# Optimization experiments

Measured on AMD Instinct MI355X. Metric: run time of the kernel, lower is better.

The kernel has to match this reference:

```python
import jax, jax.numpy as jnp
import numpy as np
import jax.ops

N_NODES = 50000
N_EDGES = 800000
N_GRAPHS = 512
F_IN = 128
HID = 256
N_CLASSES = 1

def _xavier(key, shape):
    fan_in, fan_out = shape[0], shape[1]
    std = (2.0 / (fan_in + fan_out)) ** 0.5
    return jax.random.normal(key, shape, dtype=jnp.float32) * std

def setup_inputs() -> dict:
    key = jax.random.key(0)
    ks = jax.random.split(key, 12)
    x = jax.random.normal(ks[0], (N_NODES, F_IN), dtype=jnp.float32)
    edge_index = jax.random.randint(ks[1], (2, N_EDGES), 0, N_NODES, dtype=jnp.int64)
    batch = jnp.sort(jax.random.randint(ks[2], (N_NODES,), 0, N_GRAPHS, dtype=jnp.int64))
    return {
        'x': x, 'edge_index': edge_index, 'batch': batch,
        'W0': _xavier(ks[3], (F_IN, HID)), 'b0': jnp.zeros((HID,), jnp.float32),
        'W1': _xavier(ks[4], (HID, HID)), 'b1': jnp.zeros((HID,), jnp.float32),
        'W2': _xavier(ks[5], (HID, HID)), 'b2': jnp.zeros((HID,), jnp.float32),
        'Wm1': _xavier(ks[6], (HID, HID)), 'bm1': jnp.zeros((HID,), jnp.float32),
        'Wm2': _xavier(ks[7], (HID, N_CLASSES)), 'bm2': jnp.zeros((N_CLASSES,), jnp.float32),
    }

def _gcn_layer(h, W, b, src, dst, deg_inv_sqrt):
    # PyG GCNConv: linear -> symmetric-normalized aggregation (with self loops) -> bias
    hw = h @ W                                        # [N, out]
    norm = deg_inv_sqrt[src] * deg_inv_sqrt[dst]      # [E]
    msg = hw[src] * norm[:, None]                     # [E, out]
    agg = jax.ops.segment_sum(msg, dst, num_segments=N_NODES)
    agg = agg + hw * (deg_inv_sqrt ** 2)[:, None]     # self-loop term
    return agg + b

def reference(x, edge_index, batch, W0, b0, W1, b1, W2, b2, Wm1, bm1, Wm2, bm2):
    src, dst = edge_index[0], edge_index[1]
    # degree with added self loops (in-degree at dst)
    deg = jax.ops.segment_sum(jnp.ones((N_EDGES,), jnp.float32), dst, num_segments=N_NODES) + 1.0
    deg_inv_sqrt = jax.lax.rsqrt(deg)
    h = jax.nn.relu(_gcn_layer(x, W0, b0, src, dst, deg_inv_sqrt))
    h = jax.nn.relu(_gcn_layer(h, W1, b1, src, dst, deg_inv_sqrt))
    h = jax.nn.relu(_gcn_layer(h, W2, b2, src, dst, deg_inv_sqrt))
    # global mean pool over graphs
    sums = jax.ops.segment_sum(h, batch, num_segments=N_GRAPHS)
    cnts = jax.ops.segment_sum(jnp.ones((N_NODES,), jnp.float32), batch, num_segments=N_GRAPHS)
    pooled = sums / jnp.maximum(cnts, 1.0)[:, None]   # [G, HID]
    out = jax.nn.relu(pooled @ Wm1 + bm1) @ Wm2 + bm2 # [G, num_classes]
    return out
```

## Files before the change

### kernel.cpp

```cpp
#include <hip/hip_runtime.h>

constexpr int N_NODES  = 50000;
constexpr int N_EDGES  = 800000;
constexpr int N_GRAPHS = 512;
constexpr int F_IN     = 128;
constexpr int HID      = 256;
constexpr int NPAD     = 50048;

typedef short short8 __attribute__((ext_vector_type(8)));
typedef float f32x4  __attribute__((ext_vector_type(4)));

__device__ __forceinline__ unsigned short f2b(float f) {
    unsigned u = __float_as_uint(f);
    u += 0x7fffu + ((u >> 16) & 1u);
    return (unsigned short)(u >> 16);
}
__device__ __forceinline__ float b2f_lo(unsigned u) { return __uint_as_float(u << 16); }
__device__ __forceinline__ float b2f_hi(unsigned u) { return __uint_as_float(u & 0xffff0000u); }

__global__ __launch_bounds__(256) void prep_kernel(
    const int* __restrict__ dst, int* __restrict__ deg,
    const float* __restrict__ x, unsigned short* __restrict__ x_bf,
    const float* __restrict__ W0, const float* __restrict__ W1, const float* __restrict__ W2,
    unsigned short* __restrict__ Wt0, unsigned short* __restrict__ Wt1, unsigned short* __restrict__ Wt2)
{
    const int b = blockIdx.x, t = threadIdx.x;
    if (b < 3125) {
        int e = b * 256 + t;
        atomicAdd(&deg[dst[e]], 1);
    } else if (b < 9375) {
        int i = (b - 3125) * 256 + t;
        float4 v = *reinterpret_cast<const float4*>(x + (size_t)i * 4);
        unsigned r0 = (unsigned)f2b(v.x) | ((unsigned)f2b(v.y) << 16);
        unsigned r1 = (unsigned)f2b(v.z) | ((unsigned)f2b(v.w) << 16);
        *reinterpret_cast<uint2*>(x_bf + (size_t)i * 4) = make_uint2(r0, r1);
    } else {
        int i = (b - 9375) * 256 + t;
        const float* W; unsigned short* Wt; int K; int j;
        if (i < 32768)      { W = W0; Wt = Wt0; K = 128; j = i; }
        else if (i < 98304) { W = W1; Wt = Wt1; K = 256; j = i - 32768; }
        else                { W = W2; Wt = Wt2; K = 256; j = i - 98304; }
        int k = j >> 8, n = j & 255;
        int idx = (n >> 7) * (K * 128) + (((k >> 3) * 128 + (n & 127)) << 3) + (k & 7);
        Wt[idx] = f2b(W[j]);
    }
}

__global__ void block_sum_dis_kernel(const int* __restrict__ deg, int* __restrict__ bsum,
                                     float* __restrict__ dis, int n) {
    __shared__ int sm[256];
    int t = threadIdx.x, base = blockIdx.x * 1024;
    int s = 0;
    #pragma unroll
    for (int i = 0; i < 4; ++i) {
        int idx = base + t + i * 256;
        if (idx < n) { int d = deg[idx]; s += d; dis[idx] = rsqrtf((float)d + 1.0f); }
    }
    sm[t] = s; __syncthreads();
    for (int o = 128; o > 0; o >>= 1) { if (t < o) sm[t] += sm[t + o]; __syncthreads(); }
    if (t == 0) bsum[blockIdx.x] = sm[0];
}

__global__ void scan_bsum_kernel(int* __restrict__ bsum, int nb) {
    __shared__ int sm[64];
    int t = threadIdx.x;
    int v = (t < nb) ? bsum[t] : 0;
    sm[t] = v; __syncthreads();
    for (int o = 1; o < 64; o <<= 1) {
        int a = (t >= o) ? sm[t - o] : 0; __syncthreads();
        sm[t] += a; __syncthreads();
    }
    if (t < nb) bsum[t] = sm[t] - v;
}

__global__ void scan_local_kernel(const int* __restrict__ deg, const int* __restrict__ bsum,
                                  int* __restrict__ row_start, int* __restrict__ cursor, int n) {
    __shared__ int sm[256];
    int t = threadIdx.x, base = blockIdx.x * 1024;
    int idx0 = base + t * 4;
    int v[4], s = 0;
    #pragma unroll
    for (int i = 0; i < 4; ++i) { int id = idx0 + i; v[i] = (id < n) ? deg[id] : 0; s += v[i]; }
    sm[t] = s; __syncthreads();
    for (int o = 1; o < 256; o <<= 1) {
        int a = (t >= o) ? sm[t - o] : 0; __syncthreads();
        sm[t] += a; __syncthreads();
    }
    int excl = bsum[blockIdx.x] + sm[t] - s;
    #pragma unroll
    for (int i = 0; i < 4; ++i) {
        int id = idx0 + i;
        if (id < n) { row_start[id] = excl; cursor[id] = excl; }
        excl += v[i];
    }
    if (blockIdx.x == gridDim.x - 1 && t == 255) row_start[n] = excl;
}

__global__ void fill_csr(const int* __restrict__ src, const int* __restrict__ dst,
                         const float* __restrict__ dis, int* __restrict__ cursor,
                         int2* __restrict__ csr) {
    int e = blockIdx.x * blockDim.x + threadIdx.x;
    if (e >= N_EDGES) return;
    int s = src[e], d = dst[e];
    int pos = atomicAdd(&cursor[d], 1);
    float w = dis[s] * dis[d];
    csr[pos] = make_int2(s, __float_as_int(w));
}

template<int F>
__global__ __launch_bounds__(256) void agg_bf16(
    const unsigned short* __restrict__ hin, const int* __restrict__ row_start,
    const int2* __restrict__ csr, const float* __restrict__ dis,
    uint4* __restrict__ out4)
{
    constexpr int LPR  = F / 8;
    constexpr int NSUB = 64 / LPR;
    const int lane = threadIdx.x & 63;
    const int sub  = lane / LPR;
    const int fc   = lane % LPR;
    const int node = blockIdx.x * 4 + (threadIdx.x >> 6);
    if (node >= N_NODES) return;

    float acc[8];
    {
        float dn = dis[node];
        float sw = (sub == 0) ? dn * dn : 0.0f;
        uint2 u2[2];
        *reinterpret_cast<uint4*>(u2) =
            *reinterpret_cast<const uint4*>(hin + (size_t)node * F + fc * 8);
        #pragma unroll
        for (int h = 0; h < 2; ++h) {
            acc[h * 4 + 0] = b2f_lo(u2[h].x) * sw;
            acc[h * 4 + 1] = b2f_hi(u2[h].x) * sw;
            acc[h * 4 + 2] = b2f_lo(u2[h].y) * sw;
            acc[h * 4 + 3] = b2f_hi(u2[h].y) * sw;
        }
    }

    int j = row_start[node] + sub;
    const int end = row_start[node + 1];
    for (; j + 3 * NSUB < end; j += 4 * NSUB) {
        int2 c[4];
        #pragma unroll
        for (int u = 0; u < 4; ++u) c[u] = csr[j + u * NSUB];
        #pragma unroll
        for (int u = 0; u < 4; ++u) {
            float w = __int_as_float(c[u].y);
            uint2 g[2];
            *reinterpret_cast<uint4*>(g) =
                *reinterpret_cast<const uint4*>(hin + (size_t)c[u].x * F + fc * 8);
            #pragma unroll
            for (int h = 0; h < 2; ++h) {
                acc[h * 4 + 0] = fmaf(b2f_lo(g[h].x), w, acc[h * 4 + 0]);
                acc[h * 4 + 1] = fmaf(b2f_hi(g[h].x), w, acc[h * 4 + 1]);
                acc[h * 4 + 2] = fmaf(b2f_lo(g[h].y), w, acc[h * 4 + 2]);
                acc[h * 4 + 3] = fmaf(b2f_hi(g[h].y), w, acc[h * 4 + 3]);
            }
        }
    }
    for (; j < end; j += NSUB) {
        int2 c0 = csr[j];
        float w = __int_as_float(c0.y);
        uint2 g[2];
        *reinterpret_cast<uint4*>(g) =
            *reinterpret_cast<const uint4*>(hin + (size_t)c0.x * F + fc * 8);
        #pragma unroll
        for (int h = 0; h < 2; ++h) {
            acc[h * 4 + 0] = fmaf(b2f_lo(g[h].x), w, acc[h * 4 + 0]);
            acc[h * 4 + 1] = fmaf(b2f_hi(g[h].x), w, acc[h * 4 + 1]);
            acc[h * 4 + 2] = fmaf(b2f_lo(g[h].y), w, acc[h * 4 + 2]);
            acc[h * 4 + 3] = fmaf(b2f_hi(g[h].y), w, acc[h * 4 + 3]);
        }
    }

    #pragma unroll
    for (int k = 0; k < 8; ++k) {
        #pragma unroll
        for (int off = LPR; off < 64; off <<= 1)
            acc[k] += __shfl_xor(acc[k], off, 64);
    }

    if (sub == 0) {
        uint2 r[2];
        #pragma unroll
        for (int h = 0; h < 2; ++h) {
            r[h].x = (unsigned)f2b(acc[h * 4 + 0]) | ((unsigned)f2b(acc[h * 4 + 1]) << 16);
            r[h].y = (unsigned)f2b(acc[h * 4 + 2]) | ((unsigned)f2b(acc[h * 4 + 3]) << 16);
        }
        int chunk = (node >> 7) * (128 * (F / 8)) + fc * 128 + (node & 127);
        out4[chunk] = *reinterpret_cast<uint4*>(r);
    }
}

template<int K>
__global__ __launch_bounds__(256) void gemm_frag(
    const uint4* __restrict__ A4,
    const unsigned short* __restrict__ Wt_frag,
    const float* __restrict__ bias,
    unsigned short* __restrict__ C,
    int relu)
{
    __shared__ __align__(16) unsigned short Bs[K * 128];
    const int t    = threadIdx.x;
    const int lane = t & 63;
    const int w    = t >> 6;
    const int wm   = w & 1, wn = w >> 1;
    const int q    = lane >> 4, m = lane & 15;
    const int panel = blockIdx.x;
    const int col0  = blockIdx.y * 128;

    {
        const uint4* src4 = reinterpret_cast<const uint4*>(Wt_frag + blockIdx.y * (K * 128));
        uint4* dst4 = reinterpret_cast<uint4*>(Bs);
        #pragma unroll
        for (int it = 0; it < K / 16; ++it)
            dst4[it * 256 + t] = src4[it * 256 + t];
    }
    __syncthreads();

    f32x4 acc[4][4] = {};
    const int abase = panel * (128 * (K / 8));

    #pragma unroll
    for (int kb = 0; kb < K / 32; ++kb) {
        short8 af[4], bf[4];
        #pragma unroll
        for (int i = 0; i < 4; ++i) {
            uint4 v = A4[abase + (kb * 4 + q) * 128 + wm * 64 + i * 16 + m];
            af[i] = *reinterpret_cast<short8*>(&v);
        }
        #pragma unroll
        for (int jn = 0; jn < 4; ++jn)
            bf[jn] = *reinterpret_cast<const short8*>(&Bs[((kb * 4 + q) * 128 + wn * 64 + jn * 16 + m) * 8]);
        #pragma unroll
        for (int i = 0; i < 4; ++i)
            #pragma unroll
            for (int jn = 0; jn < 4; ++jn)
                acc[i][jn] = __builtin_amdgcn_mfma_f32_16x16x32_bf16(af[i], bf[jn], acc[i][jn], 0, 0, 0);
    }

    #pragma unroll
    for (int jn = 0; jn < 4; ++jn) {
        int col = col0 + wn * 64 + jn * 16 + m;
        float bj = bias[col];
        #pragma unroll
        for (int i = 0; i < 4; ++i) {
            int rowb = panel * 128 + wm * 64 + i * 16 + q * 4;
            #pragma unroll
            for (int r = 0; r < 4; ++r) {
                float v = acc[i][jn][r] + bj;
                if (relu) v = fmaxf(v, 0.f);
                C[(size_t)(rowb + r) * 256 + col] = f2b(v);
            }
        }
    }
}

__global__ __launch_bounds__(256) void pool_mlp_kernel(
    const unsigned short* __restrict__ h, const int* __restrict__ batch,
    const float* __restrict__ Wm1, const float* __restrict__ bm1,
    const float* __restrict__ Wm2, const float* __restrict__ bm2,
    float* __restrict__ out)
{
    __shared__ float p[HID];
    __shared__ float red[HID];
    __shared__ int se[2];
    const int g = blockIdx.x, t = threadIdx.x;
    if (t < 2) {
        int target = g + t;
        int lo = 0, hi = N_NODES;
        while (lo < hi) { int mid = (lo + hi) >> 1; if (batch[mid] < target) lo = mid + 1; else hi = mid; }
        se[t] = lo;
    }
    __syncthreads();
    const int s = se[0], e = se[1];
    float acc = 0.f;
    for (int n = s; n < e; ++n) acc += b2f_lo((unsigned)h[(size_t)n * HID + t]);
    p[t] = acc / fmaxf((float)(e - s), 1.0f);
    __syncthreads();
    float a2 = bm1[t];
    for (int k = 0; k < HID; ++k) a2 = fmaf(p[k], Wm1[k * HID + t], a2);
    red[t] = fmaxf(a2, 0.f) * Wm2[t];
    __syncthreads();
    for (int o = 128; o > 0; o >>= 1) {
        if (t < o) red[t] += red[t + o];
        __syncthreads();
    }
    if (t == 0) out[g] = red[0] + bm2[0];
}

extern "C" void kernel_launch(void* const* d_in, const int* in_sizes, int n_in,
                              void* d_out, int out_size, void* d_ws, size_t ws_size,
                              hipStream_t stream) {
    const float* x    = (const float*)d_in[0];
    const int*   ei   = (const int*)d_in[1];
    const int*   batch= (const int*)d_in[2];
    const float* W0   = (const float*)d_in[3];
    const float* b0   = (const float*)d_in[4];
    const float* W1   = (const float*)d_in[5];
    const float* b1   = (const float*)d_in[6];
    const float* W2   = (const float*)d_in[7];
    const float* b2   = (const float*)d_in[8];
    const float* Wm1  = (const float*)d_in[9];
    const float* bm1  = (const float*)d_in[10];
    const float* Wm2  = (const float*)d_in[11];
    const float* bm2  = (const float*)d_in[12];
    float* out = (float*)d_out;

    char* ws = (char*)d_ws;
    size_t off = 0;
    auto alloc = [&](size_t bytes) -> void* {
        void* p = ws + off;
        off += (bytes + 255) & ~(size_t)255;
        return p;
    };
    int*   deg       = (int*)  alloc((size_t)N_NODES * 4);
    float* dis       = (float*)alloc((size_t)N_NODES * 4);
    int*   row_start = (int*)  alloc((size_t)(N_NODES + 1) * 4);
    int*   cursor    = (int*)  alloc((size_t)N_NODES * 4);
    int*   bsum      = (int*)  alloc((size_t)64 * 4);
    int2*  csr       = (int2*) alloc((size_t)N_EDGES * 8);
    unsigned short* x_bf = (unsigned short*)alloc((size_t)N_NODES * F_IN * 2);
    unsigned short* Wt0  = (unsigned short*)alloc((size_t)F_IN * HID * 2);
    unsigned short* Wt1  = (unsigned short*)alloc((size_t)HID * HID * 2);
    unsigned short* Wt2  = (unsigned short*)alloc((size_t)HID * HID * 2);
    unsigned short* bufA = (unsigned short*)alloc((size_t)NPAD * HID * 2);
    unsigned short* bufB = (unsigned short*)alloc((size_t)NPAD * HID * 2);

    const int* src = ei;
    const int* dst = ei + N_EDGES;
    const int NB = (N_NODES + 1023) / 1024;

    hipMemsetAsync(deg, 0, (size_t)N_NODES * 4, stream);
    prep_kernel         <<<10015, 256, 0, stream>>>(dst, deg, x, x_bf, W0, W1, W2, Wt0, Wt1, Wt2);
    block_sum_dis_kernel<<<NB, 256, 0, stream>>>(deg, bsum, dis, N_NODES);
    scan_bsum_kernel    <<<1, 64, 0, stream>>>(bsum, NB);
    scan_local_kernel   <<<NB, 256, 0, stream>>>(deg, bsum, row_start, cursor, N_NODES);
    fill_csr            <<<(N_EDGES + 255) / 256, 256, 0, stream>>>(src, dst, dis, cursor, csr);

    dim3 ggrid(NPAD / 128, 2);

    agg_bf16<F_IN><<<(N_NODES + 3) / 4, 256, 0, stream>>>(x_bf, row_start, csr, dis, (uint4*)bufA);
    gemm_frag<F_IN><<<ggrid, 256, 0, stream>>>((const uint4*)bufA, Wt0, b0, bufB, 1);

    agg_bf16<HID><<<(N_NODES + 3) / 4, 256, 0, stream>>>(bufB, row_start, csr, dis, (uint4*)bufA);
    gemm_frag<HID><<<ggrid, 256, 0, stream>>>((const uint4*)bufA, Wt1, b1, bufB, 1);

    agg_bf16<HID><<<(N_NODES + 3) / 4, 256, 0, stream>>>(bufB, row_start, csr, dis, (uint4*)bufA);
    gemm_frag<HID><<<ggrid, 256, 0, stream>>>((const uint4*)bufA, Wt2, b2, bufB, 1);

    pool_mlp_kernel<<<N_GRAPHS, HID, 0, stream>>>(bufB, batch, Wm1, bm1, Wm2, bm2, out);
}
```

Baseline: 430.9 us.

## Fuse neighbor aggregation and MFMA GEMM per layer via swizzled LDS tile

Merges the separate aggregation and GEMM kernels into one per-layer kernel. Each block aggregates 64 node rows into a bank-swizzled LDS tile, then multiplies that tile by the full weight matrix with MFMA, reading B fragments directly from global memory. This removes the intermediate global round-trip and three kernel launches. In exchange, each wave aggregates 16 nodes sequentially, so there is less parallelism during the gather, and weights are read from global/L2 per block instead of being staged in shared memory.

```diff
diff --git a/kernel.cpp b/kernel.cpp
--- a/kernel.cpp
+++ b/kernel.cpp
@@ -107,150 +107,140 @@
     csr[pos] = make_int2(s, __float_as_int(w));
 }
 
-template<int F>
-__global__ __launch_bounds__(256) void agg_bf16(
-    const unsigned short* __restrict__ hin, const int* __restrict__ row_start,
-    const int2* __restrict__ csr, const float* __restrict__ dis,
-    uint4* __restrict__ out4)
+template<int K>
+__global__ __launch_bounds__(256, 4) void layer_fused(
+    const unsigned short* __restrict__ hin,
+    const int* __restrict__ row_start, const int2* __restrict__ csr,
+    const float* __restrict__ dis,
+    const unsigned short* __restrict__ Wfrag,
+    const float* __restrict__ bias,
+    unsigned short* __restrict__ hout)
 {
-    constexpr int LPR  = F / 8;
+    constexpr int CPR  = K / 8;
+    constexpr int LPR  = K / 8;
     constexpr int NSUB = 64 / LPR;
-    const int lane = threadIdx.x & 63;
-    const int sub  = lane / LPR;
-    const int fc   = lane % LPR;
-    const int node = blockIdx.x * 4 + (threadIdx.x >> 6);
-    if (node >= N_NODES) return;
-
-    float acc[8];
-    {
-        float dn = dis[node];
-        float sw = (sub == 0) ? dn * dn : 0.0f;
-        uint2 u2[2];
-        *reinterpret_cast<uint4*>(u2) =
-            *reinterpret_cast<const uint4*>(hin + (size_t)node * F + fc * 8);
-        #pragma unroll
-        for (int h = 0; h < 2; ++h) {
-            acc[h * 4 + 0] = b2f_lo(u2[h].x) * sw;
-            acc[h * 4 + 1] = b2f_hi(u2[h].x) * sw;
-            acc[h * 4 + 2] = b2f_lo(u2[h].y) * sw;
-            acc[h * 4 + 3] = b2f_hi(u2[h].y) * sw;
-        }
-    }
-
-    int j = row_start[node] + sub;
-    const int end = row_start[node + 1];
-    for (; j + 3 * NSUB < end; j += 4 * NSUB) {
-        int2 c[4];
-        #pragma unroll
-        for (int u = 0; u < 4; ++u) c[u] = csr[j + u * NSUB];
-        #pragma unroll
-        for (int u = 0; u < 4; ++u) {
-            float w = __int_as_float(c[u].y);
-            uint2 g[2];
-            *reinterpret_cast<uint4*>(g) =
-                *reinterpret_cast<const uint4*>(hin + (size_t)c[u].x * F + fc * 8);
-            #pragma unroll
-            for (int h = 0; h < 2; ++h) {
-                acc[h * 4 + 0] = fmaf(b2f_lo(g[h].x), w, acc[h * 4 + 0]);
-                acc[h * 4 + 1] = fmaf(b2f_hi(g[h].x), w, acc[h * 4 + 1]);
-                acc[h * 4 + 2] = fmaf(b2f_lo(g[h].y), w, acc[h * 4 + 2]);
-                acc[h * 4 + 3] = fmaf(b2f_hi(g[h].y), w, acc[h * 4 + 3]);
-            }
-        }
-    }
-    for (; j < end; j += NSUB) {
-        int2 c0 = csr[j];
-        float w = __int_as_float(c0.y);
-        uint2 g[2];
-        *reinterpret_cast<uint4*>(g) =
-            *reinterpret_cast<const uint4*>(hin + (size_t)c0.x * F + fc * 8);
-        #pragma unroll
-        for (int h = 0; h < 2; ++h) {
-            acc[h * 4 + 0] = fmaf(b2f_lo(g[h].x), w, acc[h * 4 + 0]);
-            acc[h * 4 + 1] = fmaf(b2f_hi(g[h].x), w, acc[h * 4 + 1]);
-            acc[h * 4 + 2] = fmaf(b2f_lo(g[h].y), w, acc[h * 4 + 2]);
-            acc[h * 4 + 3] = fmaf(b2f_hi(g[h].y), w, acc[h * 4 + 3]);
-        }
-    }
-
-    #pragma unroll
-    for (int k = 0; k < 8; ++k) {
-        #pragma unroll
-        for (int off = LPR; off < 64; off <<= 1)
-            acc[k] += __shfl_xor(acc[k], off, 64);
-    }
-
-    if (sub == 0) {
-        uint2 r[2];
-        #pragma unroll
-        for (int h = 0; h < 2; ++h) {
-            r[h].x = (unsigned)f2b(acc[h * 4 + 0]) | ((unsigned)f2b(acc[h * 4 + 1]) << 16);
-            r[h].y = (unsigned)f2b(acc[h * 4 + 2]) | ((unsigned)f2b(acc[h * 4 + 3]) << 16);
-        }
-        int chunk = (node >> 7) * (128 * (F / 8)) + fc * 128 + (node & 127);
-        out4[chunk] = *reinterpret_cast<uint4*>(r);
-    }
-}
-
-template<int K>
-__global__ __launch_bounds__(256) void gemm_frag(
-    const uint4* __restrict__ A4,
-    const unsigned short* __restrict__ Wt_frag,
-    const float* __restrict__ bias,
-    unsigned short* __restrict__ C,
-    int relu)
-{
-    __shared__ __align__(16) unsigned short Bs[K * 128];
+    __shared__ __align__(16) uint4 Alds[64 * CPR];
+
     const int t    = threadIdx.x;
     const int lane = t & 63;
     const int w    = t >> 6;
-    const int wm   = w & 1, wn = w >> 1;
-    const int q    = lane >> 4, m = lane & 15;
     const int panel = blockIdx.x;
-    const int col0  = blockIdx.y * 128;
-
-    {
-        const uint4* src4 = reinterpret_cast<const uint4*>(Wt_frag + blockIdx.y * (K * 128));
-        uint4* dst4 = reinterpret_cast<uint4*>(Bs);
-        #pragma unroll
-        for (int it = 0; it < K / 16; ++it)
-            dst4[it * 256 + t] = src4[it * 256 + t];
+    const int sub  = lane / LPR;
+    const int fc   = lane % LPR;
+
+    for (int nn = 0; nn < 16; ++nn) {
+        const int r    = w * 16 + nn;
+        const int node = panel * 64 + r;
+        float acc[8];
+        if (node < N_NODES) {
+            {
+                float dn = dis[node];
+                float sw = (sub == 0) ? dn * dn : 0.0f;
+                uint2 u2[2];
+                *reinterpret_cast<uint4*>(u2) =
+                    *reinterpret_cast<const uint4*>(hin + (size_t)node * K + fc * 8);
+                #pragma unroll
+                for (int h = 0; h < 2; ++h) {
+                    acc[h * 4 + 0] = b2f_lo(u2[h].x) * sw;
+                    acc[h * 4 + 1] = b2f_hi(u2[h].x) * sw;
+                    acc[h * 4 + 2] = b2f_lo(u2[h].y) * sw;
+                    acc[h * 4 + 3] = b2f_hi(u2[h].y) * sw;
+                }
+            }
+            int j = row_start[node] + sub;
+            const int end = row_start[node + 1];
+            for (; j + 3 * NSUB < end; j += 4 * NSUB) {
+                int2 c[4];
+                #pragma unroll
+                for (int u = 0; u < 4; ++u) c[u] = csr[j + u * NSUB];
+                #pragma unroll
+                for (int u = 0; u < 4; ++u) {
+                    float wgt = __int_as_float(c[u].y);
+                    uint2 g[2];
+                    *reinterpret_cast<uint4*>(g) =
+                        *reinterpret_cast<const uint4*>(hin + (size_t)c[u].x * K + fc * 8);
+                    #pragma unroll
+                    for (int h = 0; h < 2; ++h) {
+                        acc[h * 4 + 0] = fmaf(b2f_lo(g[h].x), wgt, acc[h * 4 + 0]);
+                        acc[h * 4 + 1] = fmaf(b2f_hi(g[h].x), wgt, acc[h * 4 + 1]);
+                        acc[h * 4 + 2] = fmaf(b2f_lo(g[h].y), wgt, acc[h * 4 + 2]);
+                        acc[h * 4 + 3] = fmaf(b2f_hi(g[h].y), wgt, acc[h * 4 + 3]);
+                    }
+                }
+            }
+            for (; j < end; j += NSUB) {
+                int2 c0 = csr[j];
+                float wgt = __int_as_float(c0.y);
+                uint2 g[2];
+                *reinterpret_cast<uint4*>(g) =
+                    *reinterpret_cast<const uint4*>(hin + (size_t)c0.x * K + fc * 8);
+                #pragma unroll
+                for (int h = 0; h < 2; ++h) {
+                    acc[h * 4 + 0] = fmaf(b2f_lo(g[h].x), wgt, acc[h * 4 + 0]);
+                    acc[h * 4 + 1] = fmaf(b2f_hi(g[h].x), wgt, acc[h * 4 + 1]);
+                    acc[h * 4 + 2] = fmaf(b2f_lo(g[h].y), wgt, acc[h * 4 + 2]);
+                    acc[h * 4 + 3] = fmaf(b2f_hi(g[h].y), wgt, acc[h * 4 + 3]);
+                }
+            }
+            #pragma unroll
+            for (int k = 0; k < 8; ++k) {
+                #pragma unroll
+                for (int off = LPR; off < 64; off <<= 1)
+                    acc[k] += __shfl_xor(acc[k], off, 64);
+            }
+        } else {
+            #pragma unroll
+            for (int k = 0; k < 8; ++k) acc[k] = 0.0f;
+        }
+
+        if (sub == 0) {
+            uint2 rv[2];
+            #pragma unroll
+            for (int h = 0; h < 2; ++h) {
+                rv[h].x = (unsigned)f2b(acc[h * 4 + 0]) | ((unsigned)f2b(acc[h * 4 + 1]) << 16);
+                rv[h].y = (unsigned)f2b(acc[h * 4 + 2]) | ((unsigned)f2b(acc[h * 4 + 3]) << 16);
+            }
+            Alds[r * CPR + (fc ^ (r & 7))] = *reinterpret_cast<uint4*>(rv);
+        }
     }
     __syncthreads();
 
-    f32x4 acc[4][4] = {};
-    const int abase = panel * (128 * (K / 8));
+    const int q = lane >> 4, m = lane & 15;
+    f32x4 acc4[4][4] = {};
+    const unsigned short* bptr = Wfrag + (size_t)(w >> 1) * (K * 128);
+    const int colh = (w & 1) * 64;
 
     #pragma unroll
     for (int kb = 0; kb < K / 32; ++kb) {
+        const int kc = kb * 4 + q;
         short8 af[4], bf[4];
         #pragma unroll
         for (int i = 0; i < 4; ++i) {
-            uint4 v = A4[abase + (kb * 4 + q) * 128 + wm * 64 + i * 16 + m];
+            uint4 v = Alds[(i * 16 + m) * CPR + (kc ^ (m & 7))];
             af[i] = *reinterpret_cast<short8*>(&v);
         }
         #pragma unroll
         for (int jn = 0; jn < 4; ++jn)
-            bf[jn] = *reinterpret_cast<const short8*>(&Bs[((kb * 4 + q) * 128 + wn * 64 + jn * 16 + m) * 8]);
+            bf[jn] = *reinterpret_cast<const short8*>(&bptr[(size_t)(kc * 128 + colh + jn * 16 + m) * 8]);
         #pragma unroll
         for (int i = 0; i < 4; ++i)
             #pragma unroll
             for (int jn = 0; jn < 4; ++jn)
-                acc[i][jn] = __builtin_amdgcn_mfma_f32_16x16x32_bf16(af[i], bf[jn], acc[i][jn], 0, 0, 0);
+                acc4[i][jn] = __builtin_amdgcn_mfma_f32_16x16x32_bf16(af[i], bf[jn], acc4[i][jn], 0, 0, 0);
     }
 
     #pragma unroll
     for (int jn = 0; jn < 4; ++jn) {
-        int col = col0 + wn * 64 + jn * 16 + m;
-        float bj = bias[col];
+        const int col = w * 64 + jn * 16 + m;
+        const float bj = bias[col];
         #pragma unroll
         for (int i = 0; i < 4; ++i) {
-            int rowb = panel * 128 + wm * 64 + i * 16 + q * 4;
-            #pragma unroll
-            for (int r = 0; r < 4; ++r) {
-                float v = acc[i][jn][r] + bj;
-                if (relu) v = fmaxf(v, 0.f);
-                C[(size_t)(rowb + r) * 256 + col] = f2b(v);
+            const int rowb = panel * 64 + i * 16 + q * 4;
+            #pragma unroll
+            for (int r2 = 0; r2 < 4; ++r2) {
+                float v = acc4[i][jn][r2] + bj;
+                v = fmaxf(v, 0.f);
+                hout[(size_t)(rowb + r2) * 256 + col] = f2b(v);
             }
         }
     }
@@ -324,8 +314,8 @@
     unsigned short* Wt0  = (unsigned short*)alloc((size_t)F_IN * HID * 2);
     unsigned short* Wt1  = (unsigned short*)alloc((size_t)HID * HID * 2);
     unsigned short* Wt2  = (unsigned short*)alloc((size_t)HID * HID * 2);
-    unsigned short* bufA = (unsigned short*)alloc((size_t)NPAD * HID * 2);
-    unsigned short* bufB = (unsigned short*)alloc((size_t)NPAD * HID * 2);
+    unsigned short* h1   = (unsigned short*)alloc((size_t)NPAD * HID * 2);
+    unsigned short* h2   = (unsigned short*)alloc((size_t)NPAD * HID * 2);
 
     const int* src = ei;
     const int* dst = ei + N_EDGES;
@@ -338,16 +328,9 @@
     scan_local_kernel   <<<NB, 256, 0, stream>>>(deg, bsum, row_start, cursor, N_NODES);
     fill_csr            <<<(N_EDGES + 255) / 256, 256, 0, stream>>>(src, dst, dis, cursor, csr);
 
-    dim3 ggrid(NPAD / 128, 2);
-
-    agg_bf16<F_IN><<<(N_NODES + 3) / 4, 256, 0, stream>>>(x_bf, row_start, csr, dis, (uint4*)bufA);
-    gemm_frag<F_IN><<<ggrid, 256, 0, stream>>>((const uint4*)bufA, Wt0, b0, bufB, 1);
-
-    agg_bf16<HID><<<(N_NODES + 3) / 4, 256, 0, stream>>>(bufB, row_start, csr, dis, (uint4*)bufA);
-    gemm_frag<HID><<<ggrid, 256, 0, stream>>>((const uint4*)bufA, Wt1, b1, bufB, 1);
-
-    agg_bf16<HID><<<(N_NODES + 3) / 4, 256, 0, stream>>>(bufB, row_start, csr, dis, (uint4*)bufA);
-    gemm_frag<HID><<<ggrid, 256, 0, stream>>>((const uint4*)bufA, Wt2, b2, bufB, 1);
-
-    pool_mlp_kernel<<<N_GRAPHS, HID, 0, stream>>>(bufB, batch, Wm1, bm1, Wm2, bm2, out);
-}
+    layer_fused<F_IN><<<NPAD / 64, 256, 0, stream>>>(x_bf, row_start, csr, dis, Wt0, b0, h1);
+    layer_fused<HID> <<<NPAD / 64, 256, 0, stream>>>(h1,   row_start, csr, dis, Wt1, b1, h2);
+    layer_fused<HID> <<<NPAD / 64, 256, 0, stream>>>(h2,   row_start, csr, dis, Wt2, b2, h1);
+
+    pool_mlp_kernel<<<N_GRAPHS, HID, 0, stream>>>(h1, batch, Wm1, bm1, Wm2, bm2, out);
+}
```

After: 440.3 us. 2.2% more time.
